# Kernel optimization log

Hardware: AMD Instinct MI355X
Metric: run time of the kernel (lower is better)

## Reference

```python
import jax, jax.numpy as jnp
import numpy as np
from jax import lax

P = 192      # patches per frame
PS = 7       # patch size
GH, GW = 16, 16  # grid cells
DS = 4       # encoder downsize factor
CH = 128     # feature channels
KS, PAD = 7, 3  # harris avg-pool kernel / padding


def _encoder(x, w, b):
    # stand-in encoder: conv(1->CH, k=7, stride=DS, pad=3) + relu
    y = lax.conv_general_dilated(x, w, (DS, DS), [(PAD, PAD), (PAD, PAD)],
                                 dimension_numbers=('NCHW', 'OIHW', 'NCHW'))
    return jax.nn.relu(y + b[None, :, None, None])


def _harris(frame):
    b, n, c, h, w = frame.shape
    f = frame.reshape(b * n, c, h, w)
    dx = jnp.pad(f[..., 1:] - f[..., :-1], ((0, 0), (0, 0), (0, 0), (0, 1)), mode='reflect')
    dy = jnp.pad(f[..., 1:, :] - f[..., :-1, :], ((0, 0), (0, 0), (0, 1), (0, 0)), mode='reflect')
    def avg(x):
        s = lax.reduce_window(x, 0.0, lax.add, (1, 1, KS, KS), (1, 1, 1, 1),
                              [(0, 0), (0, 0), (PAD, PAD), (PAD, PAD)])
        return s / (KS * KS)  # count_include_pad=True like torch avg_pool2d
    Ixx, Iyy, Ixy = avg(dx * dx), avg(dy * dy), avg(dx * dy)
    return (Ixx * Iyy - Ixy * Ixy) / (Ixx + Iyy + 1e-8)


def _best_coords(g):
    bn, _, h, w = g.shape
    ph = -(-h // GH); pw = -(-w // GW)
    g = jnp.pad(g, ((0, 0), (0, 0), (0, ph * GH - h), (0, pw * GW - w)))
    g = g.reshape(bn, GH, ph, GW, pw).transpose(0, 1, 3, 2, 4).reshape(bn, GH, GW, ph * pw)
    idx = jnp.argmax(g, axis=-1)
    vals = jnp.max(g, axis=-1)
    yg = idx // pw + (ph * jnp.arange(GH))[None, :, None]
    xg = idx % pw + (pw * jnp.arange(GW))[None, None, :]
    _, top = lax.top_k(vals.reshape(bn, -1), P)
    yb = jnp.take_along_axis(yg.reshape(bn, -1), top, 1)
    xb = jnp.take_along_axis(xg.reshape(bn, -1), top, 1)
    return jnp.stack([xb, yb], -1).astype(jnp.float32)  # (bn, P, 2)


def _bilinear(img, xs, ys):
    # img (c,h,w); xs,ys (N,) pixel coords; zero padding, align_corners=False
    c, h, w = img.shape
    x0 = jnp.floor(xs); y0 = jnp.floor(ys)
    wx = xs - x0; wy = ys - y0
    x0i = x0.astype(jnp.int32); y0i = y0.astype(jnp.int32)
    out = jnp.zeros((c, xs.shape[0]), img.dtype)
    for dxi, dyi, wt in ((0, 0, (1 - wx) * (1 - wy)), (1, 0, wx * (1 - wy)),
                         (0, 1, (1 - wx) * wy), (1, 1, wx * wy)):
        xi = x0i + dxi; yi = y0i + dyi
        m = ((xi >= 0) & (xi < w) & (yi >= 0) & (yi < h)).astype(img.dtype)
        v = img[:, jnp.clip(yi, 0, h - 1), jnp.clip(xi, 0, w - 1)]
        out = out + v * (wt * m)[None, :]
    return out


def _patches(coords, fmap, cmap):
    bn, c, h, w = fmap.shape
    coords = coords / DS
    r = jnp.arange(-(PS // 2), PS // 2 + 1, dtype=jnp.float32)
    dy, dx = jnp.meshgrid(r, r, indexing='ij')
    off = jnp.stack([dx, dy], -1)                       # (PS,PS,2)
    cp = coords[:, :, None, None, :] + off[None, None]  # (bn,P,PS,PS,2)
    xp = cp[..., 0].reshape(bn, -1); yp = cp[..., 1].reshape(bn, -1)
    pf = jax.vmap(_bilinear)(fmap, xp, yp)              # (bn,c,P*PS*PS)
    pf = pf.reshape(bn, c, P, PS * PS).transpose(0, 2, 1, 3)
    pc = jax.vmap(_bilinear)(cmap, coords[..., 0], coords[..., 1])  # (bn,c,P)
    pc = pc.transpose(0, 2, 1)
    return pf, pc


def setup_inputs() -> dict:
    key = jax.random.key(0)
    k1, k2, k3 = jax.random.split(key, 3)
    frame = jax.random.uniform(k1, (4, 2, 1, 480, 640), dtype=jnp.float32)
    w_f = jax.random.normal(k2, (CH, 1, KS, KS), dtype=jnp.float32) * 0.1
    w_c = jax.random.normal(k3, (CH, 1, KS, KS), dtype=jnp.float32) * 0.1
    b_f = jnp.zeros((CH,), jnp.float32)
    b_c = jnp.zeros((CH,), jnp.float32)
    return {"frame": frame, "w_f": w_f, "b_f": b_f, "w_c": w_c, "b_c": b_c}


def reference(frame, w_f, b_f, w_c, b_c):
    b, n, c, h, w = frame.shape
    f2 = frame.reshape(b * n, c, h, w)
    fmap = _encoder(f2, w_f, b_f)
    imap = _encoder(f2, w_c, b_c)
    g = _harris(frame)
    coords = _best_coords(g)
    patches_f, patches_c = _patches(coords, fmap, imap)
    return coords, patches_f, patches_c, fmap
```

## Files before the change

kernel.cpp:

```cpp
#include <hip/hip_runtime.h>
#include <hip/hip_bf16.h>
#include <math.h>

#define BN    8
#define H     480
#define W     640
#define CH    128
#define OH    120
#define OW    160
#define P     192
#define PS    7
#define GH    16
#define GW    16
#define PH    30
#define PW    40

__global__ __launch_bounds__(256) void conv_enc(
    const float* __restrict__ f,
    const float* __restrict__ wf, const float* __restrict__ bf,
    float* __restrict__ fmap)
{
    int pix = blockIdx.x * blockDim.x + threadIdx.x;
    if (pix >= BN * OH * OW) return;
    int c0 = blockIdx.y * 16;
    int ox = pix % OW;
    int t  = pix / OW;
    int oy = t % OH;
    int b  = t / OH;

    const float* fb = f + (size_t)b * H * W;
    int iy0 = 4 * oy - 3;
    int ix0 = 4 * ox - 3;

    float in[49];
    if (oy > 0 && ox > 0) {
        #pragma unroll
        for (int ky = 0; ky < 7; ky++) {
            const float* row = fb + (iy0 + ky) * W + ix0;
            #pragma unroll
            for (int kx = 0; kx < 7; kx++) in[ky * 7 + kx] = row[kx];
        }
    } else {
        #pragma unroll
        for (int ky = 0; ky < 7; ky++) {
            int iy = iy0 + ky;
            #pragma unroll
            for (int kx = 0; kx < 7; kx++) {
                int ix = ix0 + kx;
                in[ky * 7 + kx] = (iy >= 0 && ix >= 0) ? fb[iy * W + ix] : 0.0f;
            }
        }
    }

    size_t obase = (size_t)b * CH * (OH * OW) + (size_t)oy * OW + ox;
    #pragma unroll 2
    for (int c = c0; c < c0 + 16; c++) {
        const float* wfc = wf + c * 49;
        float af = bf[c];
        #pragma unroll
        for (int k = 0; k < 49; k++) af = fmaf(wfc[k], in[k], af);
        fmap[obase + (size_t)c * (OH * OW)] = fmaxf(af, 0.0f);
    }
}

__global__ __launch_bounds__(256) void harris_cell(
    const float* __restrict__ f, float* __restrict__ cval, int* __restrict__ cidx)
{
    __shared__ float sf[37][48];
    __shared__ float dxx[36][48], dyy[36][48], dxy[36][48];
    __shared__ float sv[256];
    __shared__ int   si[256];

    int cell = blockIdx.x;
    int b  = cell >> 8;
    int ci = cell & 255;
    int gh = ci >> 4, gw = ci & 15;
    int cy0 = gh * PH, cx0 = gw * PW;
    const float* fb = f + (size_t)b * H * W;
    int tid = threadIdx.x;

    for (int i = tid; i < 37 * 47; i += 256) {
        int r = i / 47, c = i % 47;
        int y = min(max(cy0 - 3 + r, 0), H - 1);
        int x = min(max(cx0 - 3 + c, 0), W - 1);
        sf[r][c] = fb[(size_t)y * W + x];
    }
    __syncthreads();

    for (int i = tid; i < 36 * 46; i += 256) {
        int r = i / 46, c = i % 46;
        int y = cy0 - 3 + r;
        int x = cx0 - 3 + c;
        float vxx = 0.0f, vyy = 0.0f, vxy = 0.0f;
        if (y >= 0 && y < H && x >= 0 && x < W) {
            int xa = (x == W - 1) ? (x - 2) : x;
            int ya = (y == H - 1) ? (y - 2) : y;
            int lx = xa - (cx0 - 3);
            int ly = ya - (cy0 - 3);
            float dxv = sf[r][lx + 1] - sf[r][lx];
            float dyv = sf[ly + 1][c] - sf[ly][c];
            vxx = dxv * dxv;
            vyy = dyv * dyv;
            vxy = dxv * dyv;
        }
        dxx[r][c] = vxx; dyy[r][c] = vyy; dxy[r][c] = vxy;
    }
    __syncthreads();

    float best = -INFINITY;
    int   bidx = 0x7fffffff;
    for (int i = tid; i < PH * PW; i += 256) {
        int iy = i / PW, ix = i % PW;
        float Sxx = 0.0f, Syy = 0.0f, Sxy = 0.0f;
        #pragma unroll
        for (int ky = 0; ky < 7; ky++) {
            #pragma unroll
            for (int kx = 0; kx < 7; kx++) {
                Sxx += dxx[iy + ky][ix + kx];
                Syy += dyy[iy + ky][ix + kx];
                Sxy += dxy[iy + ky][ix + kx];
            }
        }
        float Ixx = Sxx / 49.0f;
        float Iyy = Syy / 49.0f;
        float Ixy = Sxy / 49.0f;
        float resp = (Ixx * Iyy - Ixy * Ixy) / (Ixx + Iyy + 1e-8f);
        if (resp > best) { best = resp; bidx = i; }
    }

    sv[tid] = best;
    si[tid] = bidx;
    __syncthreads();
    for (int s = 128; s > 0; s >>= 1) {
        if (tid < s) {
            float ov = sv[tid + s];
            int   oi = si[tid + s];
            if (ov > sv[tid] || (ov == sv[tid] && oi < si[tid])) {
                sv[tid] = ov; si[tid] = oi;
            }
        }
        __syncthreads();
    }
    if (tid == 0) { cval[cell] = sv[0]; cidx[cell] = si[0]; }
}

__global__ __launch_bounds__(256) void topk_coords(
    const float* __restrict__ cval, const int* __restrict__ cidx,
    float* __restrict__ coords)
{
    int b = blockIdx.x;
    int j = threadIdx.x;
    __shared__ float v[256];
    v[j] = cval[b * 256 + j];
    __syncthreads();
    float vj = v[j];
    int rank = 0;
    for (int k = 0; k < 256; k++) {
        float vk = v[k];
        rank += (vk > vj) || (vk == vj && k < j);
    }
    if (rank < P) {
        int ii = cidx[b * 256 + j];
        int gh = j >> 4, gw = j & 15;
        int y = ii / PW + gh * PH;
        int x = ii % PW + gw * PW;
        coords[((size_t)b * P + rank) * 2 + 0] = (float)x;
        coords[((size_t)b * P + rank) * 2 + 1] = (float)y;
    }
}

__global__ __launch_bounds__(256) void patches_kern(
    const float* __restrict__ coords,
    const float* __restrict__ fmap,
    const float* __restrict__ frame,
    const float* __restrict__ wc, const float* __restrict__ bc,
    float* __restrict__ pf, float* __restrict__ pc)
{
    __shared__ float sfm[CH][64];
    __shared__ float sf2[14][16];
    __shared__ float vq[CH][5];

    int bp = blockIdx.x;
    int b = bp / P;
    float cx = coords[(size_t)bp * 2 + 0] * 0.25f;
    float cy = coords[(size_t)bp * 2 + 1] * 0.25f;
    int tid = threadIdx.x;

    int X0 = (int)floorf(cx), Y0 = (int)floorf(cy);
    float wx = cx - (float)X0, wy = cy - (float)Y0;
    float w00 = (1.0f - wx) * (1.0f - wy);
    float w10 = wx * (1.0f - wy);
    float w01 = (1.0f - wx) * wy;
    float w11 = wx * wy;

    const float* fm = fmap + (size_t)b * CH * (OH * OW);
    for (int i = tid; i < CH * 64; i += 256) {
        int ch = i >> 6;
        int off = i & 63;
        int r = off >> 3, c = off & 7;
        int gy = Y0 - 3 + r, gx = X0 - 3 + c;
        sfm[ch][off] = (gy >= 0 && gy < OH && gx >= 0 && gx < OW)
                     ? fm[(size_t)ch * (OH * OW) + gy * OW + gx] : 0.0f;
    }

    int ix0 = 4 * X0 - 3, iy0 = 4 * Y0 - 3;
    const float* frb = frame + (size_t)b * H * W;
    for (int i = tid; i < 14 * 14; i += 256) {
        int r = i / 14, c = i % 14;
        int y = iy0 + r, x = ix0 + c;
        sf2[r][c] = (y >= 0 && y < H && x >= 0 && x < W)
                  ? frb[(size_t)y * W + x] : 0.0f;
    }
    __syncthreads();

    size_t pfbase = (size_t)bp * CH * 49;
    for (int idx = tid; idx < CH * 49; idx += 256) {
        int c = idx / 49;
        int k = idx - c * 49;
        int ky = k / 7, kx = k - ky * 7;
        int o = ky * 8 + kx;
        float acc = w00 * sfm[c][o]
                  + w10 * sfm[c][o + 1]
                  + w01 * sfm[c][o + 8]
                  + w11 * sfm[c][o + 9];
        pf[pfbase + idx] = acc;
    }

    for (int idx = tid; idx < 512; idx += 256) {
        int q = idx & 3;
        int c = idx >> 2;
        int qx = q & 1, qy = q >> 1;
        const float* wcc = wc + c * 49;
        float acc = bc[c];
        #pragma unroll
        for (int ky = 0; ky < 7; ky++) {
            #pragma unroll
            for (int kx = 0; kx < 7; kx++)
                acc = fmaf(wcc[ky * 7 + kx], sf2[4 * qy + ky][4 * qx + kx], acc);
        }
        vq[c][q] = fmaxf(acc, 0.0f);
    }
    __syncthreads();

    float m00 = (X0 >= 0 && X0 < OW && Y0 >= 0 && Y0 < OH) ? 1.0f : 0.0f;
    float m10 = (X0 + 1 >= 0 && X0 + 1 < OW && Y0 >= 0 && Y0 < OH) ? 1.0f : 0.0f;
    float m01 = (X0 >= 0 && X0 < OW && Y0 + 1 >= 0 && Y0 + 1 < OH) ? 1.0f : 0.0f;
    float m11 = (X0 + 1 >= 0 && X0 + 1 < OW && Y0 + 1 >= 0 && Y0 + 1 < OH) ? 1.0f : 0.0f;
    if (tid < CH) {
        float acc = w00 * m00 * vq[tid][0] + w10 * m10 * vq[tid][1]
                  + w01 * m01 * vq[tid][2] + w11 * m11 * vq[tid][3];
        pc[(size_t)bp * CH + tid] = acc;
    }
}

extern "C" void kernel_launch(void* const* d_in, const int* in_sizes, int n_in,
                              void* d_out, int out_size, void* d_ws, size_t ws_size,
                              hipStream_t stream)
{
    const float* frame = (const float*)d_in[0];
    const float* w_f   = (const float*)d_in[1];
    const float* b_f   = (const float*)d_in[2];
    const float* w_c   = (const float*)d_in[3];
    const float* b_c   = (const float*)d_in[4];

    float* out = (float*)d_out;
    const size_t coords_sz = (size_t)BN * P * 2;
    const size_t pf_sz     = (size_t)BN * P * CH * 49;
    const size_t pc_sz     = (size_t)BN * P * CH;
    float* coords = out;
    float* pf     = out + coords_sz;
    float* pc     = out + coords_sz + pf_sz;
    float* fmap   = out + coords_sz + pf_sz + pc_sz;

    float* cval = (float*)d_ws;
    int*   cidx = (int*)(cval + BN * 256);

    dim3 cg((BN * OH * OW) / 256, 8);
    conv_enc<<<cg, 256, 0, stream>>>(frame, w_f, b_f, fmap);

    harris_cell<<<BN * 256, 256, 0, stream>>>(frame, cval, cidx);

    topk_coords<<<BN, 256, 0, stream>>>(cval, cidx, coords);

    patches_kern<<<BN * P, 256, 0, stream>>>(
        coords, fmap, frame, w_c, b_c, pf, pc);
}
```

Measured before the change: 277.7 us.

## Reuse Harris box-filter rows across outputs and halve conv channels per block

The Harris window sum now gives each thread a column and a group of six output rows. Each loaded row of the 7-wide window is reused across all six outputs, which cuts shared-memory reads compared with recomputing the full 7x7 sum for every output. The encoder conv splits channels into 16 blocks of 8 instead of 8 blocks of 16, doubling the grid for more parallelism, at the cost of loading the input window twice as often. Tie-breaking in the per-thread argmax still picks the lowest index, because outputs are scanned in ascending order.

```diff
diff --git a/kernel.cpp b/kernel.cpp
--- a/kernel.cpp
+++ b/kernel.cpp
@@ -22,7 +22,7 @@
 {
     int pix = blockIdx.x * blockDim.x + threadIdx.x;
     if (pix >= BN * OH * OW) return;
-    int c0 = blockIdx.y * 16;
+    int c0 = blockIdx.y * 8;
     int ox = pix % OW;
     int t  = pix / OW;
     int oy = t % OH;
@@ -53,8 +53,7 @@
     }
 
     size_t obase = (size_t)b * CH * (OH * OW) + (size_t)oy * OW + ox;
-    #pragma unroll 2
-    for (int c = c0; c < c0 + 16; c++) {
+    for (int c = c0; c < c0 + 8; c++) {
         const float* wfc = wf + c * 49;
         float af = bf[c];
         #pragma unroll
@@ -109,23 +108,43 @@
 
     float best = -INFINITY;
     int   bidx = 0x7fffffff;
-    for (int i = tid; i < PH * PW; i += 256) {
-        int iy = i / PW, ix = i % PW;
-        float Sxx = 0.0f, Syy = 0.0f, Sxy = 0.0f;
-        #pragma unroll
-        for (int ky = 0; ky < 7; ky++) {
+    if (tid < 200) {
+        int col = tid % 40;
+        int grp = tid / 40;
+        int iy0 = grp * 6;
+        float axx[6] = {0,0,0,0,0,0};
+        float ayy[6] = {0,0,0,0,0,0};
+        float axy[6] = {0,0,0,0,0,0};
+        #pragma unroll
+        for (int r = 0; r < 12; r++) {
+            float vxx[7], vyy[7], vxy[7];
             #pragma unroll
             for (int kx = 0; kx < 7; kx++) {
-                Sxx += dxx[iy + ky][ix + kx];
-                Syy += dyy[iy + ky][ix + kx];
-                Sxy += dxy[iy + ky][ix + kx];
+                vxx[kx] = dxx[iy0 + r][col + kx];
+                vyy[kx] = dyy[iy0 + r][col + kx];
+                vxy[kx] = dxy[iy0 + r][col + kx];
             }
-        }
-        float Ixx = Sxx / 49.0f;
-        float Iyy = Syy / 49.0f;
-        float Ixy = Sxy / 49.0f;
-        float resp = (Ixx * Iyy - Ixy * Ixy) / (Ixx + Iyy + 1e-8f);
-        if (resp > best) { best = resp; bidx = i; }
+            #pragma unroll
+            for (int p = 0; p < 6; p++) {
+                if (r - p >= 0 && r - p <= 6) {
+                    #pragma unroll
+                    for (int kx = 0; kx < 7; kx++) {
+                        axx[p] += vxx[kx];
+                        ayy[p] += vyy[kx];
+                        axy[p] += vxy[kx];
+                    }
+                }
+            }
+        }
+        #pragma unroll
+        for (int p = 0; p < 6; p++) {
+            float Ixx = axx[p] / 49.0f;
+            float Iyy = ayy[p] / 49.0f;
+            float Ixy = axy[p] / 49.0f;
+            float resp = (Ixx * Iyy - Ixy * Ixy) / (Ixx + Iyy + 1e-8f);
+            int idx = (iy0 + p) * PW + col;
+            if (resp > best) { best = resp; bidx = idx; }
+        }
     }
 
     sv[tid] = best;
@@ -275,7 +294,7 @@
     float* cval = (float*)d_ws;
     int*   cidx = (int*)(cval + BN * 256);
 
-    dim3 cg((BN * OH * OW) / 256, 8);
+    dim3 cg((BN * OH * OW) / 256, 16);
     conv_enc<<<cg, 256, 0, stream>>>(frame, w_f, b_f, fmap);
 
     harris_cell<<<BN * 256, 256, 0, stream>>>(frame, cval, cidx);
```

After: 258.0 us. 1.08x faster.
